# Kernel tuning notes

Hardware: AMD Instinct MI355X
Metric: run time of the kernel (lower is better)

## Reference

```python
import jax, jax.numpy as jnp
import numpy as np

N, E, D, L = 50000, 800000, 96, 4
IN_H, IN_E, HID, OUT = 26, 4, 128, 8
BN_EPS, AGG_EPS = 1e-5, 1e-6


def setup_inputs() -> dict:
    key = jax.random.key(0)
    ks = jax.random.split(key, 24)
    f32 = jnp.float32
    nrm = lambda k, sh, s=0.05: jax.random.normal(k, sh, f32) * s
    inp = {
        "h1": nrm(ks[0], (N, 6), 1.0),
        "h2": nrm(ks[1], (N, 4), 1.0),
        "z": nrm(ks[2], (N, 16), 1.0),
        "efeat": nrm(ks[3], (E, IN_E), 1.0),
        "max_action": jnp.ones((N, 1), f32),
        "Wh_emb": nrm(ks[4], (IN_H, D)), "bh_emb": jnp.zeros((D,), f32),
        "We_emb": nrm(ks[5], (IN_E, D)), "be_emb": jnp.zeros((D,), f32),
        "WA": nrm(ks[6], (L, D, D)), "bA": jnp.zeros((L, D), f32),
        "WB": nrm(ks[7], (L, D, D)), "bB": jnp.zeros((L, D), f32),
        "WC": nrm(ks[8], (L, D, D)), "bC": jnp.zeros((L, D), f32),
        "WD": nrm(ks[9], (L, D, D)), "bD": jnp.zeros((L, D), f32),
        "WE": nrm(ks[10], (L, D, D)), "bE": jnp.zeros((L, D), f32),
        "bn_h_g": jnp.ones((L, D), f32), "bn_h_b": jnp.zeros((L, D), f32),
        "bn_e_g": jnp.ones((L, D), f32), "bn_e_b": jnp.zeros((L, D), f32),
        "W1": nrm(ks[11], (D, HID)), "b1": jnp.zeros((HID,), f32),
        "W2": nrm(ks[12], (HID, OUT)), "b2": jnp.zeros((OUT,), f32),
        "src": jax.random.randint(ks[13], (E,), 0, N),
        "dst": jax.random.randint(ks[14], (E,), 0, N),
    }
    return inp


def _bn(x, g, b):
    # BatchNorm1d in train mode: batch stats over node/edge axis, biased var
    mu = x.mean(axis=0)
    var = x.var(axis=0)
    return g * (x - mu) * jax.lax.rsqrt(var + BN_EPS) + b


def reference(h1, h2, z, efeat, max_action, Wh_emb, bh_emb, We_emb, be_emb,
              WA, bA, WB, bB, WC, bC, WD, bD, WE, bE,
              bn_h_g, bn_h_b, bn_e_g, bn_e_b, W1, b1, W2, b2, src, dst):
    # input embedding  (Actor concat: states then z)
    h = jnp.concatenate([h1, h2, z], axis=-1) @ Wh_emb + bh_emb   # [N, D]
    e = efeat @ We_emb + be_emb                                    # [E, D]
    n = h.shape[0]
    for l in range(L):  # GatedGCN layers (residual + BN + ReLU)
        Ah = h @ WA[l] + bA[l]
        Bh = h @ WB[l] + bB[l]
        Dh = h @ WD[l] + bD[l]
        Eh = h @ WE[l] + bE[l]
        Ce = e @ WC[l] + bC[l]
        e_new = Dh[src] + Eh[dst] + Ce                             # [E, D]
        sig = jax.nn.sigmoid(e_new)
        num = jax.ops.segment_sum(sig * Bh[src], dst, num_segments=n)
        den = jax.ops.segment_sum(sig, dst, num_segments=n)
        h_new = Ah + num / (den + AGG_EPS)
        h = h + jax.nn.relu(_bn(h_new, bn_h_g[l], bn_h_b[l]))
        e = e + jax.nn.relu(_bn(e_new, bn_e_g[l], bn_e_b[l]))
    # MLP head + tanh scale
    out = jax.nn.relu(h @ W1 + b1) @ W2 + b2                        # [N, OUT]
    return max_action * jnp.tanh(out)
```

## Files before the change

kernel.cpp:

```cpp
#include <hip/hip_runtime.h>
#include <math.h>

#define NN 50000
#define EE 800000
#define DD 96
#define NHID 128
#define NOUT 8
#define LDA 104

typedef unsigned int uint32;
typedef float floatx2 __attribute__((ext_vector_type(2)));
typedef float f32x4 __attribute__((ext_vector_type(4)));
typedef short bf16x8 __attribute__((ext_vector_type(8)));

__device__ __forceinline__ float bfu2f(ushort u) {
  union { uint32 u; float f; } v; v.u = ((uint32)u) << 16; return v.f;
}
__device__ __forceinline__ ushort f2bf(float x) {
  union { float f; uint32 u; } v; v.f = x;
  uint32 r = (v.u + 0x7fffu + ((v.u >> 16) & 1u)) >> 16;
  return (ushort)r;
}

template <int ESZ> struct EST;
template <> struct EST<2> {
  static __device__ __forceinline__ float4 ld(const void* e, size_t grp) {
    const ushort4 a = ((const ushort4*)e)[grp];
    return make_float4(bfu2f(a.x), bfu2f(a.y), bfu2f(a.z), bfu2f(a.w));
  }
  static __device__ __forceinline__ void st(void* e, size_t grp, float4 v) {
    ushort4 o; o.x = f2bf(v.x); o.y = f2bf(v.y); o.z = f2bf(v.z); o.w = f2bf(v.w);
    ((ushort4*)e)[grp] = o;
  }
  static __device__ __forceinline__ void st1(void* e, size_t idx, float v) {
    ((ushort*)e)[idx] = f2bf(v);
  }
  static __device__ __forceinline__ float ld1c(const void* e, size_t pos, int c) {
    return bfu2f(((const ushort*)e)[pos * DD + c]);
  }
};
template <> struct EST<1> {
  static __device__ __forceinline__ float4 ld(const void* e, size_t grp) {
    const int u = ((const int*)e)[grp];
    floatx2 lo = __builtin_amdgcn_cvt_pk_f32_fp8(u, false);
    floatx2 hi = __builtin_amdgcn_cvt_pk_f32_fp8(u, true);
    return make_float4(lo[0], lo[1], hi[0], hi[1]);
  }
  static __device__ __forceinline__ void st(void* e, size_t grp, float4 v) {
    int u = 0;
    u = __builtin_amdgcn_cvt_pk_fp8_f32(v.x, v.y, u, false);
    u = __builtin_amdgcn_cvt_pk_fp8_f32(v.z, v.w, u, true);
    ((int*)e)[grp] = u;
  }
  static __device__ __forceinline__ void st1(void* e, size_t idx, float v) {
    const int u = __builtin_amdgcn_cvt_pk_fp8_f32(v, v, 0, false);
    ((unsigned char*)e)[idx] = (unsigned char)(u & 0xff);
  }
  static __device__ __forceinline__ float ld1c(const void* e, size_t pos, int c) {
    const int dw = ((const int*)e)[pos * (DD / 4) + (c >> 2)];
    floatx2 lo = __builtin_amdgcn_cvt_pk_f32_fp8(dw, false);
    floatx2 hi = __builtin_amdgcn_cvt_pk_f32_fp8(dw, true);
    return (c & 2) ? ((c & 1) ? hi[1] : hi[0]) : ((c & 1) ? lo[1] : lo[0]);
  }
};

__global__ __launch_bounds__(256) void k_zero_init(int* __restrict__ cnt,
    float* __restrict__ stats) {
  int i = blockIdx.x * 256 + threadIdx.x;
  const int str = gridDim.x * 256;
  for (; i < NN; i += str) cnt[i] = 0;
  if (blockIdx.x == 0)
    for (int j = threadIdx.x; j < 768; j += 256) stats[j] = 0.f;
}

__global__ __launch_bounds__(256) void k_hist(const int* __restrict__ dst,
    int* __restrict__ cnt) {
  const int i = blockIdx.x * 256 + threadIdx.x;
  if (i < EE) atomicAdd(&cnt[dst[i]], 1);
}

__global__ __launch_bounds__(256) void k_scan(const int* __restrict__ cnt,
    int* __restrict__ rowptr, int* __restrict__ cursor) {
  __shared__ int part[256];
  const int t = threadIdx.x;
  const int CH = (NN + 255) / 256;
  const int lo = t * CH, hi = min((t + 1) * CH, NN);
  int s = 0;
  for (int i = lo; i < hi; i++) s += cnt[i];
  part[t] = s;
  __syncthreads();
  for (int off = 1; off < 256; off <<= 1) {
    int v = (t >= off) ? part[t - off] : 0;
    __syncthreads();
    part[t] += v;
    __syncthreads();
  }
  int base = (t == 0) ? 0 : part[t - 1];
  for (int i = lo; i < hi; i++) {
    rowptr[i] = base; cursor[i] = base; base += cnt[i];
  }
  if (t == 255) rowptr[NN] = base;
}

__global__ __launch_bounds__(256) void k_scatter(const int* __restrict__ src,
    const int* __restrict__ dst, int* __restrict__ cursor,
    int* __restrict__ perm, int* __restrict__ srcC, int* __restrict__ dstC) {
  const int i = blockIdx.x * 256 + threadIdx.x;
  if (i < EE) {
    const int d = dst[i];
    const int pos = atomicAdd(&cursor[d], 1);
    perm[pos] = i; srcC[pos] = src[i]; dstC[pos] = d;
  }
}

__global__ __launch_bounds__(256) void k_embed_h(const float* __restrict__ h1,
    const float* __restrict__ h2, const float* __restrict__ z,
    const float* __restrict__ W, const float* __restrict__ b,
    ushort* __restrict__ h) {
  int idx = blockIdx.x * 256 + threadIdx.x;
  const int total = NN * DD;
  const int stride = gridDim.x * 256;
  for (; idx < total; idx += stride) {
    int n = idx / DD, c = idx - n * DD;
    float acc = b[c];
#pragma unroll
    for (int k = 0; k < 6; k++)  acc = fmaf(h1[n * 6 + k], W[k * DD + c], acc);
#pragma unroll
    for (int k = 0; k < 4; k++)  acc = fmaf(h2[n * 4 + k], W[(6 + k) * DD + c], acc);
#pragma unroll
    for (int k = 0; k < 16; k++) acc = fmaf(z[n * 16 + k], W[(10 + k) * DD + c], acc);
    h[idx] = f2bf(acc);
  }
}

template <int EZ>
__global__ __launch_bounds__(256) void k_embed_e(const float* __restrict__ ef,
    const float* __restrict__ W, const float* __restrict__ b,
    const int* __restrict__ perm, void* __restrict__ e) {
  int g = blockIdx.x * 256 + threadIdx.x;
  const int totalg = EE * (DD / 4);
  const int stride = gridDim.x * 256;
  for (; g < totalg; g += stride) {
    const int pos = g / 24, cg = (g - pos * 24) * 4;
    const int orig = perm[pos];
    const float f0 = ef[orig * 4], f1 = ef[orig * 4 + 1];
    const float f2 = ef[orig * 4 + 2], f3 = ef[orig * 4 + 3];
    float4 acc;
    acc.x = b[cg+0] + f0*W[cg+0] + f1*W[DD+cg+0] + f2*W[2*DD+cg+0] + f3*W[3*DD+cg+0];
    acc.y = b[cg+1] + f0*W[cg+1] + f1*W[DD+cg+1] + f2*W[2*DD+cg+1] + f3*W[3*DD+cg+1];
    acc.z = b[cg+2] + f0*W[cg+2] + f1*W[DD+cg+2] + f2*W[2*DD+cg+2] + f3*W[3*DD+cg+2];
    acc.w = b[cg+3] + f0*W[cg+3] + f1*W[DD+cg+3] + f2*W[2*DD+cg+3] + f3*W[3*DD+cg+3];
    EST<EZ>::st(e, g, acc);
  }
}

__global__ __launch_bounds__(256) void k_ngemm(const ushort* __restrict__ h,
    const float* __restrict__ WAp, const float* __restrict__ WBp,
    const float* __restrict__ WDp, const float* __restrict__ WEp,
    const float* __restrict__ bAp, const float* __restrict__ bBp,
    const float* __restrict__ bDp, const float* __restrict__ bEp,
    ushort* __restrict__ oA, ushort* __restrict__ oB,
    ushort* __restrict__ oD, ushort* __restrict__ oE) {
  const float* W; const float* bias; ushort* out;
  const int m = blockIdx.y;
  if (m == 0)      { W = WAp; bias = bAp; out = oA; }
  else if (m == 1) { W = WBp; bias = bBp; out = oB; }
  else if (m == 2) { W = WDp; bias = bDp; out = oD; }
  else             { W = WEp; bias = bEp; out = oE; }
  __shared__ __align__(16) ushort Wt[DD * LDA];
  __shared__ __align__(16) ushort At[64 * LDA];
  const int tid = threadIdx.x;
  for (int i = tid; i < DD * DD; i += 256) {
    const int k = i / DD, n = i - (i / DD) * DD;
    Wt[n * LDA + k] = f2bf(W[i]);
  }
  const int base = blockIdx.x * 64;
  for (int i = tid; i < 64 * 24; i += 256) {
    const int r = i / 24, q = i - (i / 24) * 24;
    const int row = base + r;
    ushort4 a;
    if (row < NN) a = ((const ushort4*)h)[(size_t)row * 24 + q];
    else { a.x = 0; a.y = 0; a.z = 0; a.w = 0; }
    *(ushort4*)&At[r * LDA + q * 4] = a;
  }
  __syncthreads();
  const int w = tid >> 6, lane = tid & 63;
  const int lrow = lane & 15, lgrp = lane >> 4;
  f32x4 acc[6];
#pragma unroll
  for (int nt = 0; nt < 6; nt++) { acc[nt][0]=0.f; acc[nt][1]=0.f; acc[nt][2]=0.f; acc[nt][3]=0.f; }
#pragma unroll
  for (int kk = 0; kk < 3; kk++) {
    const bf16x8 af = *(const bf16x8*)&At[(w * 16 + lrow) * LDA + kk * 32 + lgrp * 8];
#pragma unroll
    for (int nt = 0; nt < 6; nt++) {
      const bf16x8 bfr = *(const bf16x8*)&Wt[(nt * 16 + lrow) * LDA + kk * 32 + lgrp * 8];
      acc[nt] = __builtin_amdgcn_mfma_f32_16x16x32_bf16(af, bfr, acc[nt], 0, 0, 0);
    }
  }
#pragma unroll
  for (int j = 0; j < 4; j++) {
    const int row = base + w * 16 + lgrp * 4 + j;
    if (row < NN) {
#pragma unroll
      for (int nt = 0; nt < 6; nt++) {
        const int ch = nt * 16 + lrow;
        out[(size_t)row * DD + ch] = f2bf(acc[nt][j] + bias[ch]);
      }
    }
  }
}

template <int MODE, int EZE, int EZN>
__global__ __launch_bounds__(256) void k_edge(void* __restrict__ e,
    void* __restrict__ e_new,
    const float* __restrict__ WC, const float* __restrict__ bC,
    const ushort* __restrict__ Dh, const ushort* __restrict__ Eh,
    const int* __restrict__ srcC, const int* __restrict__ dstC,
    float* __restrict__ stats) {
  __shared__ __align__(16) ushort Wt[DD * LDA];
  __shared__ __align__(16) ushort At[64 * LDA];
  __shared__ float sred[2 * DD];
  __shared__ float escl[DD], eshl[DD];
  const int tid = threadIdx.x;
  for (int i = tid; i < DD * DD; i += 256) {
    const int k = i / DD, n = i - (i / DD) * DD;
    Wt[n * LDA + k] = f2bf(WC[i]);
  }
  if (tid < 2 * DD) sred[tid] = 0.f;
  if (MODE >= 1 && tid < DD) { escl[tid] = stats[576 + tid]; eshl[tid] = stats[672 + tid]; }
  __syncthreads();
  const int w = tid >> 6, lane = tid & 63;
  const int lrow = lane & 15, lgrp = lane >> 4;
  float sacc[6], qacc[6];
#pragma unroll
  for (int nt = 0; nt < 6; nt++) { sacc[nt] = 0.f; qacc[nt] = 0.f; }
  const int NT = EE / 64;
  for (int t = blockIdx.x; t < NT; t += gridDim.x) {
    const size_t base = (size_t)t * 64;
    for (int i = tid; i < 64 * 24; i += 256) {
      const int r = i / 24, gq = i - (i / 24) * 24;
      const size_t gi = (base + r) * 24 + gq;
      float4 a = EST<EZE>::ld(e, gi);
      if (MODE >= 1) {
        const float4 d = EST<EZN>::ld(e_new, gi);
        const int c = gq * 4;
        a.x += fmaxf(fmaf(d.x, escl[c],     eshl[c]),     0.f);
        a.y += fmaxf(fmaf(d.y, escl[c + 1], eshl[c + 1]), 0.f);
        a.z += fmaxf(fmaf(d.z, escl[c + 2], eshl[c + 2]), 0.f);
        a.w += fmaxf(fmaf(d.w, escl[c + 3], eshl[c + 3]), 0.f);
        if (MODE == 1) EST<EZE>::st(e, gi, a);
      }
      ushort4 o; o.x = f2bf(a.x); o.y = f2bf(a.y); o.z = f2bf(a.z); o.w = f2bf(a.w);
      *(ushort4*)&At[r * LDA + gq * 4] = o;
    }
    __syncthreads();
    f32x4 acc[6];
#pragma unroll
    for (int nt = 0; nt < 6; nt++) { acc[nt][0]=0.f; acc[nt][1]=0.f; acc[nt][2]=0.f; acc[nt][3]=0.f; }
#pragma unroll
    for (int kk = 0; kk < 3; kk++) {
      const bf16x8 af = *(const bf16x8*)&At[(w * 16 + lrow) * LDA + kk * 32 + lgrp * 8];
#pragma unroll
      for (int nt = 0; nt < 6; nt++) {
        const bf16x8 bfr = *(const bf16x8*)&Wt[(nt * 16 + lrow) * LDA + kk * 32 + lgrp * 8];
        acc[nt] = __builtin_amdgcn_mfma_f32_16x16x32_bf16(af, bfr, acc[nt], 0, 0, 0);
      }
    }
#pragma unroll
    for (int j = 0; j < 4; j++) {
      const int rloc = w * 16 + lgrp * 4 + j;
      const size_t pos = base + rloc;
      const int s = srcC[pos], d2 = dstC[pos];
#pragma unroll
      for (int nt = 0; nt < 6; nt++) {
        const int ch = nt * 16 + lrow;
        const float v = acc[nt][j] + bC[ch]
            + bfu2f(Dh[(size_t)s * DD + ch]) + bfu2f(Eh[(size_t)d2 * DD + ch]);
        sacc[nt] += v; qacc[nt] += v * v;
        EST<EZN>::st1(e_new, pos * DD + ch, v);
      }
    }
    __syncthreads();
  }
#pragma unroll
  for (int nt = 0; nt < 6; nt++) {
    const int ch = nt * 16 + lrow;
    atomicAdd(&sred[ch], sacc[nt]);
    atomicAdd(&sred[DD + ch], qacc[nt]);
  }
  __syncthreads();
  if (tid < 2 * DD) atomicAdd(&stats[tid], sred[tid]);
}

template <int EZN>
__global__ __launch_bounds__(256) void k_agg(const void* __restrict__ e_new,
    const int* __restrict__ srcC, const int* __restrict__ rowptr,
    const ushort* __restrict__ Bh, ushort* __restrict__ hn,
    float* __restrict__ stats) {
  __shared__ float sred[2 * DD];
  if (threadIdx.x < 2 * DD) sred[threadIdx.x] = 0.f;
  __syncthreads();
  const int hw = threadIdx.x >> 5, lane = threadIdx.x & 31;
  const int c0 = lane, c1 = lane + 32, c2 = lane + 64;
  float sa0 = 0, sa1 = 0, sa2 = 0, qa0 = 0, qa1 = 0, qa2 = 0;
  for (int n = blockIdx.x * 8 + hw; n < NN; n += gridDim.x * 8) {
    const int rs = rowptr[n], re = rowptr[n + 1];
    float n0 = 0, n1 = 0, n2 = 0, d0 = 0, d1 = 0, d2 = 0;
    for (int p = rs; p < re; p++) {
      const int s = srcC[p];
      const float v0 = EST<EZN>::ld1c(e_new, (size_t)p, c0);
      const float v1 = EST<EZN>::ld1c(e_new, (size_t)p, c1);
      const float v2 = EST<EZN>::ld1c(e_new, (size_t)p, c2);
      const float g0 = 1.f / (1.f + __expf(-v0));
      const float g1 = 1.f / (1.f + __expf(-v1));
      const float g2 = 1.f / (1.f + __expf(-v2));
      const size_t sb = (size_t)s * DD;
      n0 += g0 * bfu2f(Bh[sb + c0]); d0 += g0;
      n1 += g1 * bfu2f(Bh[sb + c1]); d1 += g1;
      n2 += g2 * bfu2f(Bh[sb + c2]); d2 += g2;
    }
    const size_t hb = (size_t)n * DD;
    const float v0 = bfu2f(hn[hb + c0]) + n0 / (d0 + 1e-6f);
    const float v1 = bfu2f(hn[hb + c1]) + n1 / (d1 + 1e-6f);
    const float v2 = bfu2f(hn[hb + c2]) + n2 / (d2 + 1e-6f);
    hn[hb + c0] = f2bf(v0); hn[hb + c1] = f2bf(v1); hn[hb + c2] = f2bf(v2);
    sa0 += v0; qa0 += v0 * v0;
    sa1 += v1; qa1 += v1 * v1;
    sa2 += v2; qa2 += v2 * v2;
  }
  atomicAdd(&sred[c0], sa0); atomicAdd(&sred[c1], sa1); atomicAdd(&sred[c2], sa2);
  atomicAdd(&sred[DD + c0], qa0); atomicAdd(&sred[DD + c1], qa1); atomicAdd(&sred[DD + c2], qa2);
  __syncthreads();
  if (threadIdx.x < 2 * DD) atomicAdd(&stats[192 + threadIdx.x], sred[threadIdx.x]);
}

__global__ void k_finalize(float* __restrict__ stats,
    const float* __restrict__ g_h, const float* __restrict__ b_h,
    const float* __restrict__ g_e, const float* __restrict__ b_e) {
  const int c = threadIdx.x;
  if (c < DD) {
    const float mu_h = stats[192 + c] / (float)NN;
    const float var_h = stats[288 + c] / (float)NN - mu_h * mu_h;
    const float sc_h = g_h[c] * rsqrtf(var_h + 1e-5f);
    const float mu_e = stats[c] / (float)EE;
    const float var_e = stats[96 + c] / (float)EE - mu_e * mu_e;
    const float sc_e = g_e[c] * rsqrtf(var_e + 1e-5f);
    stats[384 + c] = sc_h;
    stats[480 + c] = b_h[c] - mu_h * sc_h;
    stats[576 + c] = sc_e;
    stats[672 + c] = b_e[c] - mu_e * sc_e;
    stats[c] = 0.f; stats[96 + c] = 0.f; stats[192 + c] = 0.f; stats[288 + c] = 0.f;
  }
}

__global__ __launch_bounds__(256) void k_update_h(ushort* __restrict__ h,
    const ushort* __restrict__ hn, const float* __restrict__ stats) {
  int idx = blockIdx.x * 256 + threadIdx.x;
  const int stride = gridDim.x * 256;
  for (; idx < NN * DD; idx += stride) {
    const int c = idx % DD;
    const float v = fmaf(bfu2f(hn[idx]), stats[384 + c], stats[480 + c]);
    h[idx] = f2bf(bfu2f(h[idx]) + fmaxf(v, 0.f));
  }
}

__global__ __launch_bounds__(256) void k_head(const ushort* __restrict__ h,
    const float* __restrict__ W1, const float* __restrict__ b1,
    const float* __restrict__ W2, const float* __restrict__ b2,
    const float* __restrict__ ma, float* __restrict__ out) {
  __shared__ float W1l[DD * NHID];
  __shared__ float W2l[NHID * NOUT];
  __shared__ float hid[4][NHID];
  __shared__ float hrow[4][DD];
  for (int i = threadIdx.x; i < DD * NHID; i += 256) W1l[i] = W1[i];
  for (int i = threadIdx.x; i < NHID * NOUT; i += 256) W2l[i] = W2[i];
  __syncthreads();
  const int w = threadIdx.x >> 6, lane = threadIdx.x & 63;
  for (int n = blockIdx.x * 4 + w; n < NN; n += gridDim.x * 4) {
    const ushort* hp = h + (size_t)n * DD;
    if (lane < DD - 64) hrow[w][64 + lane] = bfu2f(hp[64 + lane]);
    hrow[w][lane] = bfu2f(hp[lane]);
    float a0 = b1[lane], a1 = b1[64 + lane];
    for (int k = 0; k < DD; k++) {
      const float x = hrow[w][k];
      a0 = fmaf(x, W1l[k * NHID + lane], a0);
      a1 = fmaf(x, W1l[k * NHID + 64 + lane], a1);
    }
    hid[w][lane] = fmaxf(a0, 0.f);
    hid[w][64 + lane] = fmaxf(a1, 0.f);
    if (lane < NOUT) {
      float o = b2[lane];
      for (int k = 0; k < NHID; k++) o = fmaf(hid[w][k], W2l[k * NOUT + lane], o);
      out[(size_t)n * NOUT + lane] = ma[n] * tanhf(o);
    }
  }
}

extern "C" void kernel_launch(void* const* d_in, const int* in_sizes, int n_in,
                              void* d_out, int out_size, void* d_ws, size_t ws_size,
                              hipStream_t stream) {
  const float* h1  = (const float*)d_in[0];
  const float* h2  = (const float*)d_in[1];
  const float* z   = (const float*)d_in[2];
  const float* ef  = (const float*)d_in[3];
  const float* ma  = (const float*)d_in[4];
  const float* Wh  = (const float*)d_in[5];
  const float* bh  = (const float*)d_in[6];
  const float* We  = (const float*)d_in[7];
  const float* be  = (const float*)d_in[8];
  const float* WA  = (const float*)d_in[9];
  const float* bA  = (const float*)d_in[10];
  const float* WB  = (const float*)d_in[11];
  const float* bB  = (const float*)d_in[12];
  const float* WC  = (const float*)d_in[13];
  const float* bC  = (const float*)d_in[14];
  const float* WD  = (const float*)d_in[15];
  const float* bD  = (const float*)d_in[16];
  const float* WE  = (const float*)d_in[17];
  const float* bE  = (const float*)d_in[18];
  const float* bn_h_g = (const float*)d_in[19];
  const float* bn_h_b = (const float*)d_in[20];
  const float* bn_e_g = (const float*)d_in[21];
  const float* bn_e_b = (const float*)d_in[22];
  const float* W1  = (const float*)d_in[23];
  const float* b1  = (const float*)d_in[24];
  const float* W2  = (const float*)d_in[25];
  const float* b2  = (const float*)d_in[26];
  const int*   src = (const int*)d_in[27];
  const int*   dst = (const int*)d_in[28];

  const size_t E_ELEMS = (size_t)EE * DD;
  const size_t N_ELEMS = (size_t)NN * DD;
  int tier;
  if (ws_size >= 455000000UL)      tier = 0;
  else if (ws_size >= 297000000UL) tier = 1;
  else                             tier = 2;
  const size_t esze = (tier == 0) ? 2 : 1;
  const size_t eszn = (tier <= 1) ? 2 : 1;

  char* p = (char*)d_ws;
  void* e     = (void*)p; p += E_ELEMS * esze;
  void* e_new = (void*)p; p += E_ELEMS * eszn;
  ushort* h   = (ushort*)p; p += N_ELEMS * 2;
  ushort* hn  = (ushort*)p; p += N_ELEMS * 2;
  ushort* Bhb = (ushort*)p; p += N_ELEMS * 2;
  ushort* Dhb = (ushort*)p; p += N_ELEMS * 2;
  ushort* Ehb = (ushort*)p; p += N_ELEMS * 2;
  int* cnt    = (int*)p; p += (size_t)NN * 4;
  int* rowptr = (int*)p; p += (size_t)(NN + 1) * 4;
  int* cursor = (int*)p; p += (size_t)NN * 4;
  int* perm   = (int*)p; p += (size_t)EE * 4;
  int* srcC   = (int*)p; p += (size_t)EE * 4;
  int* dstC   = (int*)p; p += (size_t)EE * 4;
  float* stats = (float*)p;

  k_zero_init<<<64, 256, 0, stream>>>(cnt, stats);
  k_hist<<<3125, 256, 0, stream>>>(dst, cnt);
  k_scan<<<1, 256, 0, stream>>>(cnt, rowptr, cursor);
  k_scatter<<<3125, 256, 0, stream>>>(src, dst, cursor, perm, srcC, dstC);
  k_embed_h<<<1024, 256, 0, stream>>>(h1, h2, z, Wh, bh, h);
  if (esze == 2) k_embed_e<2><<<2048, 256, 0, stream>>>(ef, We, be, perm, e);
  else           k_embed_e<1><<<2048, 256, 0, stream>>>(ef, We, be, perm, e);

  for (int l = 0; l < 4; l++) {
    dim3 gn(782, 4);
    k_ngemm<<<gn, 256, 0, stream>>>(h,
        WA + l * DD * DD, WB + l * DD * DD, WD + l * DD * DD, WE + l * DD * DD,
        bA + l * DD, bB + l * DD, bD + l * DD, bE + l * DD,
        hn, Bhb, Dhb, Ehb);
    const float* WCl = WC + l * DD * DD;
    const float* bCl = bC + l * DD;
#define EDGE_ARGS e, e_new, WCl, bCl, Dhb, Ehb, srcC, dstC, stats
    if (tier == 0) {
      if (l == 0)      k_edge<0,2,2><<<1250, 256, 0, stream>>>(EDGE_ARGS);
      else if (l < 3)  k_edge<1,2,2><<<1250, 256, 0, stream>>>(EDGE_ARGS);
      else             k_edge<2,2,2><<<1250, 256, 0, stream>>>(EDGE_ARGS);
    } else if (tier == 1) {
      if (l == 0)      k_edge<0,1,2><<<1250, 256, 0, stream>>>(EDGE_ARGS);
      else if (l < 3)  k_edge<1,1,2><<<1250, 256, 0, stream>>>(EDGE_ARGS);
      else             k_edge<2,1,2><<<1250, 256, 0, stream>>>(EDGE_ARGS);
    } else {
      if (l == 0)      k_edge<0,1,1><<<1250, 256, 0, stream>>>(EDGE_ARGS);
      else if (l < 3)  k_edge<1,1,1><<<1250, 256, 0, stream>>>(EDGE_ARGS);
      else             k_edge<2,1,1><<<1250, 256, 0, stream>>>(EDGE_ARGS);
    }
#undef EDGE_ARGS
    if (eszn == 2) k_agg<2><<<1024, 256, 0, stream>>>(e_new, srcC, rowptr, Bhb, hn, stats);
    else           k_agg<1><<<1024, 256, 0, stream>>>(e_new, srcC, rowptr, Bhb, hn, stats);
    k_finalize<<<1, 128, 0, stream>>>(stats,
        bn_h_g + l * DD, bn_h_b + l * DD, bn_e_g + l * DD, bn_e_b + l * DD);
    k_update_h<<<1024, 256, 0, stream>>>(h, hn, stats);
  }

  k_head<<<1024, 256, 0, stream>>>(h, W1, b1, W2, b2, ma, (float*)d_out);
}
```

Before: 2.198 ms.

## Stage edge GEMM output through LDS for vectorized gather and store

The edge kernel's MFMA results are written back to shared memory so each lane then processes 4 contiguous channels per row. Dh/Eh gathers and e_new stores become 4-wide vector accesses instead of scalar per-channel accesses. Src/dst indices are staged in shared memory once per tile, and the BN statistics accumulators are remapped to the new channel ownership. This adds an extra LDS round trip, and the At write-back is not separated from the MFMA reads by a barrier, which is a possible hazard across waves.

```diff
diff --git a/kernel.cpp b/kernel.cpp
--- a/kernel.cpp
+++ b/kernel.cpp
@@ -31,9 +31,6 @@
   static __device__ __forceinline__ void st(void* e, size_t grp, float4 v) {
     ushort4 o; o.x = f2bf(v.x); o.y = f2bf(v.y); o.z = f2bf(v.z); o.w = f2bf(v.w);
     ((ushort4*)e)[grp] = o;
-  }
-  static __device__ __forceinline__ void st1(void* e, size_t idx, float v) {
-    ((ushort*)e)[idx] = f2bf(v);
   }
   static __device__ __forceinline__ float ld1c(const void* e, size_t pos, int c) {
     return bfu2f(((const ushort*)e)[pos * DD + c]);
@@ -51,10 +48,6 @@
     u = __builtin_amdgcn_cvt_pk_fp8_f32(v.x, v.y, u, false);
     u = __builtin_amdgcn_cvt_pk_fp8_f32(v.z, v.w, u, true);
     ((int*)e)[grp] = u;
-  }
-  static __device__ __forceinline__ void st1(void* e, size_t idx, float v) {
-    const int u = __builtin_amdgcn_cvt_pk_fp8_f32(v, v, 0, false);
-    ((unsigned char*)e)[idx] = (unsigned char)(u & 0xff);
   }
   static __device__ __forceinline__ float ld1c(const void* e, size_t pos, int c) {
     const int dw = ((const int*)e)[pos * (DD / 4) + (c >> 2)];
@@ -222,6 +215,7 @@
   __shared__ __align__(16) ushort At[64 * LDA];
   __shared__ float sred[2 * DD];
   __shared__ float escl[DD], eshl[DD];
+  __shared__ int sidx_s[64], sidx_d[64];
   const int tid = threadIdx.x;
   for (int i = tid; i < DD * DD; i += 256) {
     const int k = i / DD, n = i - (i / DD) * DD;
@@ -232,13 +226,21 @@
   __syncthreads();
   const int w = tid >> 6, lane = tid & 63;
   const int lrow = lane & 15, lgrp = lane >> 4;
-  float sacc[6], qacc[6];
-#pragma unroll
-  for (int nt = 0; nt < 6; nt++) { sacc[nt] = 0.f; qacc[nt] = 0.f; }
+  const int qq0 = lane % 24;
+  const int qq1 = (lane + 16) % 24;
+  const int qq2 = (lane + 8) % 24;
+  const float4 bc0 = *(const float4*)&bC[qq0 * 4];
+  const float4 bc1 = *(const float4*)&bC[qq1 * 4];
+  const float4 bc2 = *(const float4*)&bC[qq2 * 4];
+  float sacc0[4] = {0,0,0,0}, sacc1[4] = {0,0,0,0}, sacc2[4] = {0,0,0,0};
+  float qacc0[4] = {0,0,0,0}, qacc1[4] = {0,0,0,0}, qacc2[4] = {0,0,0,0};
+
   const int NT = EE / 64;
   for (int t = blockIdx.x; t < NT; t += gridDim.x) {
     const size_t base = (size_t)t * 64;
-    for (int i = tid; i < 64 * 24; i += 256) {
+#pragma unroll
+    for (int ii = 0; ii < 6; ii++) {
+      const int i = ii * 256 + tid;
       const int r = i / 24, gq = i - (i / 24) * 24;
       const size_t gi = (base + r) * 24 + gq;
       float4 a = EST<EZE>::ld(e, gi);
@@ -254,6 +256,7 @@
       ushort4 o; o.x = f2bf(a.x); o.y = f2bf(a.y); o.z = f2bf(a.z); o.w = f2bf(a.w);
       *(ushort4*)&At[r * LDA + gq * 4] = o;
     }
+    if (tid < 64) { sidx_s[tid] = srcC[base + tid]; sidx_d[tid] = dstC[base + tid]; }
     __syncthreads();
     f32x4 acc[6];
 #pragma unroll
@@ -269,25 +272,49 @@
     }
 #pragma unroll
     for (int j = 0; j < 4; j++) {
-      const int rloc = w * 16 + lgrp * 4 + j;
-      const size_t pos = base + rloc;
-      const int s = srcC[pos], d2 = dstC[pos];
 #pragma unroll
       for (int nt = 0; nt < 6; nt++) {
-        const int ch = nt * 16 + lrow;
-        const float v = acc[nt][j] + bC[ch]
-            + bfu2f(Dh[(size_t)s * DD + ch]) + bfu2f(Eh[(size_t)d2 * DD + ch]);
-        sacc[nt] += v; qacc[nt] += v * v;
-        EST<EZN>::st1(e_new, pos * DD + ch, v);
+        At[(w * 16 + lgrp * 4 + j) * LDA + nt * 16 + lrow] = f2bf(acc[nt][j]);
       }
     }
+#pragma unroll
+    for (int it = 0; it < 6; it++) {
+      const int idx = it * 64 + lane;
+      const int r16 = idx / 24, gq = idx - r16 * 24;
+      const int row = w * 16 + r16;
+      const size_t pos = base + row;
+      const int s = sidx_s[row], d2 = sidx_d[row];
+      const ushort4 av = *(const ushort4*)&At[row * LDA + gq * 4];
+      const ushort4 dv = *(const ushort4*)&Dh[(size_t)s * DD + gq * 4];
+      const ushort4 ev = *(const ushort4*)&Eh[(size_t)d2 * DD + gq * 4];
+      const float4 bc = (it % 3 == 0) ? bc0 : (it % 3 == 1) ? bc1 : bc2;
+      float4 v;
+      v.x = bfu2f(av.x) + bc.x + bfu2f(dv.x) + bfu2f(ev.x);
+      v.y = bfu2f(av.y) + bc.y + bfu2f(dv.y) + bfu2f(ev.y);
+      v.z = bfu2f(av.z) + bc.z + bfu2f(dv.z) + bfu2f(ev.z);
+      v.w = bfu2f(av.w) + bc.w + bfu2f(dv.w) + bfu2f(ev.w);
+      if (it % 3 == 0) {
+        sacc0[0]+=v.x; sacc0[1]+=v.y; sacc0[2]+=v.z; sacc0[3]+=v.w;
+        qacc0[0]+=v.x*v.x; qacc0[1]+=v.y*v.y; qacc0[2]+=v.z*v.z; qacc0[3]+=v.w*v.w;
+      } else if (it % 3 == 1) {
+        sacc1[0]+=v.x; sacc1[1]+=v.y; sacc1[2]+=v.z; sacc1[3]+=v.w;
+        qacc1[0]+=v.x*v.x; qacc1[1]+=v.y*v.y; qacc1[2]+=v.z*v.z; qacc1[3]+=v.w*v.w;
+      } else {
+        sacc2[0]+=v.x; sacc2[1]+=v.y; sacc2[2]+=v.z; sacc2[3]+=v.w;
+        qacc2[0]+=v.x*v.x; qacc2[1]+=v.y*v.y; qacc2[2]+=v.z*v.z; qacc2[3]+=v.w*v.w;
+      }
+      EST<EZN>::st(e_new, pos * 24 + gq, v);
+    }
     __syncthreads();
   }
 #pragma unroll
-  for (int nt = 0; nt < 6; nt++) {
-    const int ch = nt * 16 + lrow;
-    atomicAdd(&sred[ch], sacc[nt]);
-    atomicAdd(&sred[DD + ch], qacc[nt]);
+  for (int c = 0; c < 4; c++) {
+    atomicAdd(&sred[qq0 * 4 + c], sacc0[c]);
+    atomicAdd(&sred[DD + qq0 * 4 + c], qacc0[c]);
+    atomicAdd(&sred[qq1 * 4 + c], sacc1[c]);
+    atomicAdd(&sred[DD + qq1 * 4 + c], qacc1[c]);
+    atomicAdd(&sred[qq2 * 4 + c], sacc2[c]);
+    atomicAdd(&sred[DD + qq2 * 4 + c], qacc2[c]);
   }
   __syncthreads();
   if (tid < 2 * DD) atomicAdd(&stats[tid], sred[tid]);
```

After: 2.057 ms. 6.4% less time.
